# Optimization experiments

Measured on AMD Instinct MI355X. Metric: run time of the kernel, lower is better.

Reference implementation:

```python
import jax, jax.numpy as jnp
import numpy as np

N, E, NC, F0, MID = 20000, 320000, 16, 67, 32
Y0 = 0.28209479177387814   # 1/(2*sqrt(pi)), real spherical harmonic l=0
C1 = 0.4886025119029199    # sqrt(3/(4*pi)),  real spherical harmonic l=1 coeff


def setup_inputs() -> dict:
    key = jax.random.key(0)
    ks = jax.random.split(key, 16)
    rn = lambda k, shape, s=1.0: jax.random.normal(k, shape, dtype=jnp.float32) * s
    return {
        "node_feats": rn(ks[0], (N, F0)),
        "pos": rn(ks[1], (N, 3)) * 3.0,
        "edge_w": jax.random.uniform(ks[2], (E, 2), dtype=jnp.float32),
        "lin1_W": rn(ks[5], (F0, F0), 1.0 / np.sqrt(F0)),
        "lin1_b": jnp.zeros((F0,), jnp.float32),
        "lin2_W": rn(ks[6], (F0, NC), 1.0 / np.sqrt(F0)),
        "lin2_b": jnp.zeros((NC,), jnp.float32),
        # 4 radial nets = 2 GConv layers x 2 degree pairs ((0,0),(0,1))
        "rW1": rn(ks[7], (4, 3, MID), 1.0 / np.sqrt(3)),
        "rb1": jnp.zeros((4, MID), jnp.float32),
        "ln1_g": jnp.ones((4, MID), jnp.float32),
        "ln1_b": jnp.zeros((4, MID), jnp.float32),
        "rW2": rn(ks[8], (4, MID, MID), 1.0 / np.sqrt(MID)),
        "rb2": jnp.zeros((4, MID), jnp.float32),
        "ln2_g": jnp.ones((4, MID), jnp.float32),
        "ln2_b": jnp.zeros((4, MID), jnp.float32),
        "rW3": rn(ks[9], (4, MID, NC * NC), 1.0 / np.sqrt(MID)),
        "rb3": jnp.zeros((4, NC * NC), jnp.float32),
        "Wself": rn(ks[10], (2, NC, NC), 1.0 / np.sqrt(NC)),
        "src": jax.random.randint(ks[3], (E,), 0, N),
        "dst": jax.random.randint(ks[4], (E,), 0, N),
    }


def _layer_norm(x, g, b, eps=1e-5):
    mu = jnp.mean(x, -1, keepdims=True)
    var = jnp.mean((x - mu) ** 2, -1, keepdims=True)
    return (x - mu) * jax.lax.rsqrt(var + eps) * g + b


def _forward(node_feats, pos, edge_w, lin1_W, lin1_b, lin2_W, lin2_b,
             rW1, rb1, ln1_g, ln1_b, rW2, rb2, ln2_g, ln2_b, rW3, rb3,
             Wself, src, dst):
    # node embedding: Linear -> ELU -> (dropout p=0) -> Linear -> [N, NC]
    h0 = jax.nn.elu(node_feats @ lin1_W + lin1_b) @ lin2_W + lin2_b

    # get_basis_and_r: relative positions, radial distance, SH basis (d_in=0)
    d = pos[dst] - pos[src]                                   # [E, 3]
    r = jnp.sqrt(jnp.sum(d * d, -1))                          # [E]
    rhat = d / jnp.maximum(r, 1e-8)[:, None]
    Y1 = C1 * rhat[:, jnp.array([1, 2, 0])]                   # [E, 3] (y, z, x order)
    feat = jnp.concatenate([edge_w, r[:, None]], -1)          # [E, edge_dim+1=3]

    deg = jax.ops.segment_sum(jnp.ones((E,), feat.dtype), dst, num_segments=N)
    inv_deg = jnp.where(deg > 0, 1.0 / jnp.maximum(deg, 1.0), 0.0)
    has_in = (deg > 0).astype(feat.dtype)

    def radial(i):
        h = jnp.maximum(_layer_norm(feat @ rW1[i] + rb1[i], ln1_g[i], ln1_b[i]), 0.0)
        h = jnp.maximum(_layer_norm(h @ rW2[i] + rb2[i], ln2_g[i], ln2_b[i]), 0.0)
        return (h @ rW3[i] + rb3[i]).reshape(E, NC, NC)       # [E, nc_out, nc_in]

    out1 = None
    for li in range(2):  # faithful to source bug: both layers read only degree-0 feats
        R00 = radial(2 * li)        # pairwise kernel (0->0), num_freq=1
        R01 = radial(2 * li + 1)    # pairwise kernel (0->1), num_freq=1
        s = h0[src]                                           # [E, NC] gather
        msg0 = Y0 * jnp.einsum('eoi,ei->eo', R00, s)          # [E, NC]
        msg1 = jnp.einsum('eoi,ei,em->eom', R01, s, Y1)       # [E, NC, 3]
        out0 = jax.ops.segment_sum(msg0, dst, num_segments=N) * inv_deg[:, None]
        out0 = out0 + has_in[:, None] * (h0 @ Wself[li].T)    # self-interaction (deg 0)
        out1 = jax.ops.segment_sum(msg1, dst, num_segments=N) * inv_deg[:, None, None]
        h0 = out0
    return h0[:, :, None], out1                               # {'0': [N,NC,1], '1': [N,NC,3]}


def reference(node_feats, pos, edge_w, lin1_W, lin1_b, lin2_W, lin2_b,
              rW1, rb1, ln1_g, ln1_b, rW2, rb2, ln2_g, ln2_b, rW3, rb3,
              Wself, src, dst):
    return _forward(node_feats, pos, edge_w, lin1_W, lin1_b, lin2_W, lin2_b,
                    rW1, rb1, ln1_g, ln1_b, rW2, rb2, ln2_g, ln2_b, rW3, rb3,
                    Wself, src, dst)
```

## Files before the change

### kernel.cpp

```cpp
#include <hip/hip_runtime.h>
#include <hip/hip_fp16.h>


#define Y0C 0.28209479177387814f
#define C1C 0.4886025119029199f

typedef _Float16 hv2 __attribute__((ext_vector_type(2)));

#if defined(__has_builtin)
#if __has_builtin(__builtin_amdgcn_fdot2)
#define FDOT2(a, b, c) __builtin_amdgcn_fdot2((a), (b), (c), false)
#endif
#endif
#ifndef FDOT2
#define FDOT2(a, b, c) ((c) + (float)(a).x * (float)(b).x + (float)(a).y * (float)(b).y)
#endif

static __device__ __forceinline__ unsigned h2u(__half2 h) {
    union { __half2 h; unsigned u; } x; x.h = h; return x.u;
}
static __device__ __forceinline__ __half2 u2h(unsigned u) {
    union { unsigned u; __half2 h; } x; x.u = u; return x.h;
}
static __device__ __forceinline__ hv2 u2hv(unsigned u) {
    union { unsigned u; hv2 h; } x; x.u = u; return x.h;
}
static __device__ __forceinline__ unsigned hv2u(hv2 h) {
    union { hv2 h; unsigned u; } x; x.h = h; return x.u;
}
static __device__ __forceinline__ hv2 f2hv(float a, float b) {
    hv2 r; r.x = (_Float16)a; r.y = (_Float16)b; return r;
}
static __device__ __forceinline__ float hbits2f(unsigned short s) {
    __half_raw r; r.x = s; return __half2float((__half)r);
}

struct RadialW {
    const float *W1, *b1, *g1, *gb1, *b2, *g2, *gb2;
    const unsigned* W2q;
};

__device__ __forceinline__ void radial_net_pk(float x0, float x1, float x2,
                                              RadialW rw, hv2* hvpk ) {
    float h[32];
#pragma unroll
    for (int j = 0; j < 32; ++j)
        h[j] = rw.b1[j] + x0 * rw.W1[j] + x1 * rw.W1[32 + j] + x2 * rw.W1[64 + j];
    float s0 = 0.f, s1 = 0.f, s2 = 0.f, s3 = 0.f;
#pragma unroll
    for (int p = 0; p < 8; ++p) {
        s0 += h[4 * p]; s1 += h[4 * p + 1]; s2 += h[4 * p + 2]; s3 += h[4 * p + 3];
    }
    float mu = ((s0 + s1) + (s2 + s3)) * 0.03125f;
    float v0 = 0.f, v1 = 0.f, v2 = 0.f, v3 = 0.f;
#pragma unroll
    for (int p = 0; p < 8; ++p) {
        float d0 = h[4 * p] - mu, d1 = h[4 * p + 1] - mu;
        float d2 = h[4 * p + 2] - mu, d3 = h[4 * p + 3] - mu;
        v0 = fmaf(d0, d0, v0); v1 = fmaf(d1, d1, v1);
        v2 = fmaf(d2, d2, v2); v3 = fmaf(d3, d3, v3);
    }
    float var = ((v0 + v1) + (v2 + v3)) * 0.03125f;
    float rs = rsqrtf(var + 1e-5f);
#pragma unroll
    for (int j = 0; j < 32; ++j)
        h[j] = fmaxf((h[j] - mu) * rs * rw.g1[j] + rw.gb1[j], 0.f);

    hv2 hp[16];
#pragma unroll
    for (int p = 0; p < 16; ++p) hp[p] = f2hv(h[2 * p], h[2 * p + 1]);

    float h2[32];
#pragma unroll
    for (int j = 0; j < 32; ++j) {
        float acc = rw.b2[j];
        const unsigned* __restrict__ wj = rw.W2q + j * 16;
#pragma unroll
        for (int kp = 0; kp < 16; ++kp)
            acc = FDOT2(hp[kp], u2hv(wj[kp]), acc);
        h2[j] = acc;
    }
    s0 = s1 = s2 = s3 = 0.f;
#pragma unroll
    for (int p = 0; p < 8; ++p) {
        s0 += h2[4 * p]; s1 += h2[4 * p + 1]; s2 += h2[4 * p + 2]; s3 += h2[4 * p + 3];
    }
    mu = ((s0 + s1) + (s2 + s3)) * 0.03125f;
    v0 = v1 = v2 = v3 = 0.f;
#pragma unroll
    for (int p = 0; p < 8; ++p) {
        float d0 = h2[4 * p] - mu, d1 = h2[4 * p + 1] - mu;
        float d2 = h2[4 * p + 2] - mu, d3 = h2[4 * p + 3] - mu;
        v0 = fmaf(d0, d0, v0); v1 = fmaf(d1, d1, v1);
        v2 = fmaf(d2, d2, v2); v3 = fmaf(d3, d3, v3);
    }
    var = ((v0 + v1) + (v2 + v3)) * 0.03125f;
    rs = rsqrtf(var + 1e-5f);
    float y[32];
#pragma unroll
    for (int j = 0; j < 32; ++j)
        y[j] = fmaxf((h2[j] - mu) * rs * rw.g2[j] + rw.gb2[j], 0.f);
#pragma unroll
    for (int p = 0; p < 16; ++p) hvpk[p] = f2hv(y[2 * p], y[2 * p + 1]);
}

__device__ __forceinline__ void contract_dot(const hv2* hvpk,
                                             const uint4* __restrict__ Um,
                                             const float* __restrict__ Ut,
                                             float* v ) {
    float4 t0 = ((const float4*)Ut)[0];
    float4 t1 = ((const float4*)Ut)[1];
    float4 t2 = ((const float4*)Ut)[2];
    float4 t3 = ((const float4*)Ut)[3];
    float tail[16] = {t0.x, t0.y, t0.z, t0.w, t1.x, t1.y, t1.z, t1.w,
                      t2.x, t2.y, t2.z, t2.w, t3.x, t3.y, t3.z, t3.w};
#pragma unroll
    for (int o = 0; o < 16; ++o) {
        uint4 q0 = Um[o * 4];
        uint4 q1 = Um[o * 4 + 1];
        uint4 q2 = Um[o * 4 + 2];
        uint4 q3 = Um[o * 4 + 3];
        float acc = tail[o];
        acc = FDOT2(hvpk[0],  u2hv(q0.x), acc);
        acc = FDOT2(hvpk[1],  u2hv(q0.y), acc);
        acc = FDOT2(hvpk[2],  u2hv(q0.z), acc);
        acc = FDOT2(hvpk[3],  u2hv(q0.w), acc);
        acc = FDOT2(hvpk[4],  u2hv(q1.x), acc);
        acc = FDOT2(hvpk[5],  u2hv(q1.y), acc);
        acc = FDOT2(hvpk[6],  u2hv(q1.z), acc);
        acc = FDOT2(hvpk[7],  u2hv(q1.w), acc);
        acc = FDOT2(hvpk[8],  u2hv(q2.x), acc);
        acc = FDOT2(hvpk[9],  u2hv(q2.y), acc);
        acc = FDOT2(hvpk[10], u2hv(q2.z), acc);
        acc = FDOT2(hvpk[11], u2hv(q2.w), acc);
        acc = FDOT2(hvpk[12], u2hv(q3.x), acc);
        acc = FDOT2(hvpk[13], u2hv(q3.y), acc);
        acc = FDOT2(hvpk[14], u2hv(q3.z), acc);
        acc = FDOT2(hvpk[15], u2hv(q3.w), acc);
        v[o] = acc;
    }
}

__global__ __launch_bounds__(256) void k_embed1(
    const float* __restrict__ nf, const float* __restrict__ W1,
    const float* __restrict__ b1, float* __restrict__ t, int N, int nbEmb,
    const float* __restrict__ rW3, const float* __restrict__ rW2,
    unsigned* __restrict__ Wp, unsigned* __restrict__ Wq) {
    if (blockIdx.x >= (unsigned)nbEmb) {
        int tt = (blockIdx.x - nbEmb) * 256 + threadIdx.x;
        if (tt < 3 * 256) {
            int ni = tt >> 8;
            int net = (ni == 0) ? 0 : ni + 1;
            int r = tt & 255;
            int i = r >> 4, o = r & 15;
            const float* __restrict__ W3n = rW3 + (size_t)net * 8192;
            unsigned* __restrict__ dp = Wp + (size_t)ni * 4608 + (size_t)(i * 16 + o) * 18;
#pragma unroll
            for (int kp = 0; kp < 16; ++kp) {
                float a = W3n[(2 * kp) * 256 + o * 16 + i];
                float b = W3n[(2 * kp + 1) * 256 + o * 16 + i];
                dp[kp] = h2u(__floats2half2_rn(a, b));
            }
        } else if (tt < 3 * 256 + 3 * 512) {
            int r = tt - 3 * 256;
            int ni = r / 512;
            int net = (ni == 0) ? 0 : ni + 1;
            int jk = r - ni * 512;
            int j = jk >> 4, kp = jk & 15;
            const float* __restrict__ W2n = rW2 + (size_t)net * 1024;
            Wq[ni * 512 + j * 16 + kp] =
                h2u(__floats2half2_rn(W2n[(2 * kp) * 32 + j],
                                      W2n[(2 * kp + 1) * 32 + j]));
        }
        return;
    }
    int idx = blockIdx.x * 256 + threadIdx.x;
    if (idx >= N * 67) return;
    int n = idx / 67, j = idx - n * 67;
    const float* __restrict__ x = nf + (size_t)n * 67;
    const float* __restrict__ w = W1 + j;
    float a0 = b1[j], a1 = 0.f, a2 = 0.f, a3 = 0.f;
#pragma unroll
    for (int i = 0; i < 64; i += 4) {
        a0 = fmaf(x[i],     w[(size_t)i * 67],       a0);
        a1 = fmaf(x[i + 1], w[(size_t)(i + 1) * 67], a1);
        a2 = fmaf(x[i + 2], w[(size_t)(i + 2) * 67], a2);
        a3 = fmaf(x[i + 3], w[(size_t)(i + 3) * 67], a3);
    }
    a0 = fmaf(x[64], w[64 * 67], a0);
    a1 = fmaf(x[65], w[65 * 67], a1);
    a2 = fmaf(x[66], w[66 * 67], a2);
    float s = (a0 + a1) + (a2 + a3);
    t[idx] = (s > 0.f) ? s : expm1f(s);
}

__global__ __launch_bounds__(256) void k_embed2(
    const float* __restrict__ t, const float* __restrict__ W2,
    const float* __restrict__ b2, float* __restrict__ h0, int N) {
    int idx = blockIdx.x * 256 + threadIdx.x;
    if (idx >= N * 16) return;
    int n = idx >> 4, c = idx & 15;
    const float* __restrict__ x = t + (size_t)n * 67;
    const float* __restrict__ w = W2 + c;
    float a0 = b2[c], a1 = 0.f, a2 = 0.f, a3 = 0.f;
#pragma unroll
    for (int i = 0; i < 64; i += 4) {
        a0 = fmaf(x[i],     w[(size_t)i * 16],       a0);
        a1 = fmaf(x[i + 1], w[(size_t)(i + 1) * 16], a1);
        a2 = fmaf(x[i + 2], w[(size_t)(i + 2) * 16], a2);
        a3 = fmaf(x[i + 3], w[(size_t)(i + 3) * 16], a3);
    }
    a0 = fmaf(x[64], w[64 * 16], a0);
    a1 = fmaf(x[65], w[65 * 16], a1);
    a2 = fmaf(x[66], w[66 * 16], a2);
    h0[idx] = (a0 + a1) + (a2 + a3);
}

__global__ void k_count2(const int* __restrict__ src, const int* __restrict__ dst,
                         int* __restrict__ cntd, int* __restrict__ cnts,
                         int* __restrict__ posd, int* __restrict__ poss, int E) {
    int e = blockIdx.x * blockDim.x + threadIdx.x;
    if (e >= E) return;
    posd[e] = atomicAdd(cntd + dst[e], 1);
    poss[e] = atomicAdd(cnts + src[e], 1);
}

__global__ __launch_bounds__(1024) void k_scan2(const int* __restrict__ cntd,
                                                int* __restrict__ rsd,
                                                const int* __restrict__ cnts,
                                                int* __restrict__ rss, int N) {
    const int* __restrict__ c = (blockIdx.x == 0) ? cntd : cnts;
    int* __restrict__ rs      = (blockIdx.x == 0) ? rsd  : rss;
    int chunk = (N + 1023) >> 10;
    int lo = (int)threadIdx.x * chunk;
    int sum = 0;
    for (int j = 0; j < chunk; ++j) { int i = lo + j; sum += (i < N) ? c[i] : 0; }
    __shared__ int ps[1024];
    ps[threadIdx.x] = sum;
    __syncthreads();
    for (int off = 1; off < 1024; off <<= 1) {
        int t = (threadIdx.x >= (unsigned)off) ? ps[threadIdx.x - off] : 0;
        __syncthreads();
        ps[threadIdx.x] += t;
        __syncthreads();
    }
    int run = threadIdx.x ? ps[threadIdx.x - 1] : 0;
    if (threadIdx.x == 0) rs[0] = 0;
    for (int j = 0; j < chunk; ++j) {
        int i = lo + j;
        if (i < N) { run += c[i]; rs[i + 1] = run; }
    }
}

__global__ void k_prep(const float* __restrict__ pos, const float* __restrict__ ew,
                       const int* __restrict__ src, const int* __restrict__ dst,
                       const int* __restrict__ rsd, const int* __restrict__ rss,
                       const int* __restrict__ posd, const int* __restrict__ poss,
                       float4* __restrict__ edgeS, uint2* __restrict__ y1d,
                       int* __restrict__ s2d, int E) {
    int e = blockIdx.x * blockDim.x + threadIdx.x;
    if (e >= E) return;
    int s = src[e], d = dst[e];
    float dx = pos[3 * d]     - pos[3 * s];
    float dy = pos[3 * d + 1] - pos[3 * s + 1];
    float dz = pos[3 * d + 2] - pos[3 * s + 2];
    float r = sqrtf(dx * dx + dy * dy + dz * dz);
    float im = 1.f / fmaxf(r, 1e-8f);
    int ts = rss[s] + poss[e];
    int td = rsd[d] + posd[e];
    s2d[ts] = td;
    edgeS[ts] = make_float4(ew[2 * e], ew[2 * e + 1], r, __int_as_float(s));
    y1d[td] = make_uint2(h2u(__floats2half2_rn(C1C * dy * im, C1C * dz * im)),
                         h2u(__floats2half2_rn(C1C * dx * im, 0.f)));
}

__global__ __launch_bounds__(256) void k_u2(
    const float* __restrict__ h, const unsigned* __restrict__ Wp,
    const float* __restrict__ b3A, const float* __restrict__ b3B,
    unsigned* __restrict__ Um0, float* __restrict__ Ut0,
    unsigned* __restrict__ Um1, float* __restrict__ Ut1,
    int wpA, int nbPerNet, int N) {
    __shared__ unsigned WL[4608];
    int netSel = blockIdx.x / nbPerNet;
    int nbase = (blockIdx.x - netSel * nbPerNet) * 32;
    const unsigned* __restrict__ g = Wp + (size_t)(wpA + netSel) * 4608;
    for (int j = threadIdx.x; j < 4608; j += 256) WL[j] = g[j];
    __syncthreads();

    const float* __restrict__ b3 = netSel ? b3B : b3A;
    unsigned* __restrict__ Um = netSel ? Um1 : Um0;
    float*    __restrict__ Ut = netSel ? Ut1 : Ut0;

    int o = threadIdx.x & 15;
    int pr = threadIdx.x >> 4;
    int n0 = nbase + pr * 2;
    int n1 = n0 + 1;
    bool ok0 = n0 < N, ok1 = n1 < N;
    int m0 = ok0 ? n0 : 0, m1 = ok1 ? n1 : 0;

    const float* __restrict__ bo = b3 + o * 16;
    float tA = 0.f, tB = 0.f;
    __half2 hhA[16], hhB[16];
    {
        const float4* hp = (const float4*)(h + (size_t)m0 * 16);
#pragma unroll
        for (int q = 0; q < 4; ++q) {
            float4 hv = hp[q];
            tA += hv.x * bo[4 * q] + hv.y * bo[4 * q + 1]
                + hv.z * bo[4 * q + 2] + hv.w * bo[4 * q + 3];
            hhA[4 * q]     = __floats2half2_rn(hv.x, hv.x);
            hhA[4 * q + 1] = __floats2half2_rn(hv.y, hv.y);
            hhA[4 * q + 2] = __floats2half2_rn(hv.z, hv.z);
            hhA[4 * q + 3] = __floats2half2_rn(hv.w, hv.w);
        }
    }
    {
        const float4* hp = (const float4*)(h + (size_t)m1 * 16);
#pragma unroll
        for (int q = 0; q < 4; ++q) {
            float4 hv = hp[q];
            tB += hv.x * bo[4 * q] + hv.y * bo[4 * q + 1]
                + hv.z * bo[4 * q + 2] + hv.w * bo[4 * q + 3];
            hhB[4 * q]     = __floats2half2_rn(hv.x, hv.x);
            hhB[4 * q + 1] = __floats2half2_rn(hv.y, hv.y);
            hhB[4 * q + 2] = __floats2half2_rn(hv.z, hv.z);
            hhB[4 * q + 3] = __floats2half2_rn(hv.w, hv.w);
        }
    }

    __half2 accA[16], accB[16];
#pragma unroll
    for (int p = 0; p < 16; ++p) {
        accA[p] = __floats2half2_rn(0.f, 0.f);
        accB[p] = __floats2half2_rn(0.f, 0.f);
    }

#pragma unroll
    for (int i = 0; i < 16; ++i) {
        const uint2* __restrict__ row = (const uint2*)(WL + i * 288 + o * 18);
        __half2 ha = hhA[i], hb = hhB[i];
#pragma unroll
        for (int q = 0; q < 8; ++q) {
            uint2 w = row[q];
            accA[2 * q]     = __hfma2(ha, u2h(w.x), accA[2 * q]);
            accA[2 * q + 1] = __hfma2(ha, u2h(w.y), accA[2 * q + 1]);
            accB[2 * q]     = __hfma2(hb, u2h(w.x), accB[2 * q]);
            accB[2 * q + 1] = __hfma2(hb, u2h(w.y), accB[2 * q + 1]);
        }
    }

    if (ok0) {
        uint4* du = (uint4*)(Um + ((size_t)(n0 * 16 + o)) * 16);
#pragma unroll
        for (int q = 0; q < 4; ++q)
            du[q] = make_uint4(h2u(accA[4 * q]), h2u(accA[4 * q + 1]),
                               h2u(accA[4 * q + 2]), h2u(accA[4 * q + 3]));
        Ut[n0 * 16 + o] = tA;
    }
    if (ok1) {
        uint4* du = (uint4*)(Um + ((size_t)(n1 * 16 + o)) * 16);
#pragma unroll
        for (int q = 0; q < 4; ++q)
            du[q] = make_uint4(h2u(accB[4 * q]), h2u(accB[4 * q + 1]),
                               h2u(accB[4 * q + 2]), h2u(accB[4 * q + 3]));
        Ut[n1 * 16 + o] = tB;
    }
}

__global__ __launch_bounds__(256) void k_edgeL0(
    const float4* __restrict__ edgeS, const int* __restrict__ s2d, RadialW ra,
    const uint4* __restrict__ UmA, const float* __restrict__ UtA,
    unsigned short* __restrict__ msg , int E) {
    int t = blockIdx.x * blockDim.x + threadIdx.x;
    if (t >= E) return;
    float4 a = edgeS[t];
    int sn = __float_as_int(a.w);
    hv2 hv[16];
    float v[16];
    radial_net_pk(a.x, a.y, a.z, ra, hv);
    contract_dot(hv, UmA + (size_t)sn * 64, UtA + (size_t)sn * 16, v);
    int td = s2d[t];
    uint4* m = (uint4*)(msg + (size_t)td * 16);
    m[0] = make_uint4(hv2u(f2hv(v[0], v[1])),  hv2u(f2hv(v[2], v[3])),
                      hv2u(f2hv(v[4], v[5])),  hv2u(f2hv(v[6], v[7])));
    m[1] = make_uint4(hv2u(f2hv(v[8], v[9])),  hv2u(f2hv(v[10], v[11])),
                      hv2u(f2hv(v[12], v[13])), hv2u(f2hv(v[14], v[15])));
}

__global__ __launch_bounds__(256) void k_edgeL1(
    const float4* __restrict__ edgeS, const int* __restrict__ s2d,
    RadialW ra, RadialW rb,
    const uint4* __restrict__ UmA, const float* __restrict__ UtA,
    const uint4* __restrict__ UmB, const float* __restrict__ UtB,
    unsigned short* __restrict__ msg , int nbE, int E) {
    int half = (blockIdx.x >= (unsigned)nbE) ? 1 : 0;
    int t = (blockIdx.x - half * nbE) * blockDim.x + threadIdx.x;
    if (t >= E) return;
    float4 a = edgeS[t];
    int sn = __float_as_int(a.w);
    RadialW rw = half ? rb : ra;
    const uint4* __restrict__ Um = half ? UmB : UmA;
    const float* __restrict__ Ut = half ? UtB : UtA;
    hv2 hv[16];
    float v[16];
    radial_net_pk(a.x, a.y, a.z, rw, hv);
    contract_dot(hv, Um + (size_t)sn * 64, Ut + (size_t)sn * 16, v);
    int td = s2d[t];
    uint4* m = (uint4*)(msg + (size_t)td * 32 + half * 16);
    m[0] = make_uint4(hv2u(f2hv(v[0], v[1])),  hv2u(f2hv(v[2], v[3])),
                      hv2u(f2hv(v[4], v[5])),  hv2u(f2hv(v[6], v[7])));
    m[1] = make_uint4(hv2u(f2hv(v[8], v[9])),  hv2u(f2hv(v[10], v[11])),
                      hv2u(f2hv(v[12], v[13])), hv2u(f2hv(v[14], v[15])));
}

__global__ void k_reduce0(const unsigned short* __restrict__ msg,
                          const int* __restrict__ rowstart,
                          const float* __restrict__ h, const float* __restrict__ Wself,
                          float* __restrict__ out, int N) {
    int idx = blockIdx.x * blockDim.x + threadIdx.x;
    if (idx >= N * 16) return;
    int n = idx >> 4, o = idx & 15;
    int s = rowstart[n], t1 = rowstart[n + 1];
    float acc0 = 0.f, acc1 = 0.f;
    int t = s;
    for (; t + 1 < t1; t += 2) {
        acc0 += hbits2f(msg[(size_t)t * 16 + o]);
        acc1 += hbits2f(msg[(size_t)(t + 1) * 16 + o]);
    }
    if (t < t1) acc0 += hbits2f(msg[(size_t)t * 16 + o]);
    float acc = acc0 + acc1;
    int d = t1 - s;
    float invd = (d > 0) ? 1.f / (float)d : 0.f;
    float hi   = (d > 0) ? 1.f : 0.f;
    const float* __restrict__ hn = h + (size_t)n * 16;
    const float* __restrict__ w  = Wself + o * 16;
    float self = 0.f;
#pragma unroll
    for (int c = 0; c < 16; ++c) self += hn[c] * w[c];
    out[idx] = Y0C * acc * invd + hi * self;
}

__global__ void k_reduce1(const unsigned short* __restrict__ msg,
                          const uint2* __restrict__ y1d,
                          const int* __restrict__ rowstart,
                          const float* __restrict__ h, const float* __restrict__ Wself,
                          float* __restrict__ out0, float* __restrict__ out1, int N) {
    int idx = blockIdx.x * blockDim.x + threadIdx.x;
    if (idx >= N * 16) return;
    int n = idx >> 4, o = idx & 15;
    int s = rowstart[n], t1 = rowstart[n + 1];
    float a0 = 0.f, ax = 0.f, ay = 0.f, az = 0.f;
    float b0 = 0.f, bx = 0.f, by = 0.f, bz = 0.f;
    int t = s;
    for (; t + 1 < t1; t += 2) {
        const unsigned short* rowA = msg + (size_t)t * 32;
        const unsigned short* rowB = msg + (size_t)(t + 1) * 32;
        uint2 yva = y1d[t];
        uint2 yvb = y1d[t + 1];
        a0 += hbits2f(rowA[o]);
        b0 += hbits2f(rowB[o]);
        float pa = hbits2f(rowA[16 + o]);
        float pb = hbits2f(rowB[16 + o]);
        ax = fmaf(pa, hbits2f((unsigned short)yva.x), ax);
        ay = fmaf(pa, hbits2f((unsigned short)(yva.x >> 16)), ay);
        az = fmaf(pa, hbits2f((unsigned short)yva.y), az);
        bx = fmaf(pb, hbits2f((unsigned short)yvb.x), bx);
        by = fmaf(pb, hbits2f((unsigned short)(yvb.x >> 16)), by);
        bz = fmaf(pb, hbits2f((unsigned short)yvb.y), bz);
    }
    if (t < t1) {
        const unsigned short* rowA = msg + (size_t)t * 32;
        uint2 yva = y1d[t];
        a0 += hbits2f(rowA[o]);
        float pa = hbits2f(rowA[16 + o]);
        ax = fmaf(pa, hbits2f((unsigned short)yva.x), ax);
        ay = fmaf(pa, hbits2f((unsigned short)(yva.x >> 16)), ay);
        az = fmaf(pa, hbits2f((unsigned short)yva.y), az);
    }
    a0 += b0; ax += bx; ay += by; az += bz;
    int d = t1 - s;
    float invd = (d > 0) ? 1.f / (float)d : 0.f;
    float hi   = (d > 0) ? 1.f : 0.f;
    const float* __restrict__ hn = h + (size_t)n * 16;
    const float* __restrict__ w  = Wself + o * 16;
    float self = 0.f;
#pragma unroll
    for (int c = 0; c < 16; ++c) self += hn[c] * w[c];
    out0[idx] = Y0C * a0 * invd + hi * self;
    out1[(size_t)idx * 3]     = ax * invd;
    out1[(size_t)idx * 3 + 1] = ay * invd;
    out1[(size_t)idx * 3 + 2] = az * invd;
}

extern "C" void kernel_launch(void* const* d_in, const int* in_sizes, int n_in,
                              void* d_out, int out_size, void* d_ws, size_t ws_size,
                              hipStream_t stream) {
    (void)n_in; (void)out_size; (void)ws_size;
    const float* node_feats = (const float*)d_in[0];
    const float* pos    = (const float*)d_in[1];
    const float* edge_w = (const float*)d_in[2];
    const float* lin1_W = (const float*)d_in[3];
    const float* lin1_b = (const float*)d_in[4];
    const float* lin2_W = (const float*)d_in[5];
    const float* lin2_b = (const float*)d_in[6];
    const float* rW1    = (const float*)d_in[7];
    const float* rb1    = (const float*)d_in[8];
    const float* ln1_g  = (const float*)d_in[9];
    const float* ln1_b  = (const float*)d_in[10];
    const float* rW2    = (const float*)d_in[11];
    const float* rb2    = (const float*)d_in[12];
    const float* ln2_g  = (const float*)d_in[13];
    const float* ln2_b  = (const float*)d_in[14];
    const float* rW3    = (const float*)d_in[15];
    const float* rb3    = (const float*)d_in[16];
    const float* Wself  = (const float*)d_in[17];
    const int*   src    = (const int*)d_in[18];
    const int*   dst    = (const int*)d_in[19];

    const int N = in_sizes[1] / 3;
    const int E = in_sizes[18];

    char* ws = (char*)d_ws;
    size_t off = 0;
    auto carve = [&](size_t bytes) -> char* {
        char* p = ws + off;
        off = (off + bytes + 255) & ~(size_t)255;
        return p;
    };
    float* h0   = (float*)carve((size_t)N * 16 * 4);
    float* h1   = (float*)carve((size_t)N * 16 * 4);
    int*   cntd = (int*)carve((size_t)N * 4);
    int*   cnts = (int*)carve((size_t)N * 4);
    int*   rsd  = (int*)carve((size_t)(N + 1) * 4);
    int*   rss  = (int*)carve((size_t)(N + 1) * 4);
    int*   s2d  = (int*)carve((size_t)E * 4);
    float4* edgeS = (float4*)carve((size_t)E * 16);
    uint2*  y1d   = (uint2*)carve((size_t)E * 8);
    unsigned* UaM = (unsigned*)carve((size_t)N * 16 * 64);
    float*    UaT = (float*)carve((size_t)N * 16 * 4);
    unsigned* UbM = (unsigned*)carve((size_t)N * 16 * 64);
    float*    UbT = (float*)carve((size_t)N * 16 * 4);
    unsigned* Wp  = (unsigned*)carve((size_t)3 * 4608 * 4);
    unsigned* Wq  = (unsigned*)carve((size_t)3 * 512 * 4);
    unsigned short* msg = (unsigned short*)carve((size_t)E * 32 * 2);
    float* tmb = (float*)msg;
    int* posd = (int*)((char*)msg + (8u << 20));
    int* poss = (int*)((char*)msg + (14u << 20));

    auto nb = [](int n) { return (n + 255) / 256; };
    const int nbE = nb(E);
    const int nbU = (N + 31) / 32;
    const int nbE1 = nb(N * 67);

    hipMemsetAsync(cntd, 0, (size_t)((char*)cnts - (char*)cntd) + (size_t)N * 4, stream);

    k_embed1<<<nbE1 + 9, 256, 0, stream>>>(node_feats, lin1_W, lin1_b, tmb, N,
                                           nbE1, rW3, rW2, Wp, Wq);
    k_embed2<<<nb(N * 16), 256, 0, stream>>>(tmb, lin2_W, lin2_b, h0, N);

    k_count2<<<nbE, 256, 0, stream>>>(src, dst, cntd, cnts, posd, poss, E);
    k_scan2<<<2, 1024, 0, stream>>>(cntd, rsd, cnts, rss, N);
    k_prep<<<nbE, 256, 0, stream>>>(pos, edge_w, src, dst, rsd, rss, posd, poss,
                                    edgeS, y1d, s2d, E);

    auto rnet = [&](int net, int ni) -> RadialW {
        RadialW r;
        r.W1 = rW1 + net * 96;   r.b1 = rb1 + net * 32;
        r.g1 = ln1_g + net * 32; r.gb1 = ln1_b + net * 32;
        r.b2 = rb2 + net * 32;
        r.g2 = ln2_g + net * 32; r.gb2 = ln2_b + net * 32;
        r.W2q = Wq + ni * 512;
        return r;
    };

    k_u2<<<nbU, 256, 0, stream>>>(h0, Wp, rb3, rb3, UaM, UaT, UbM, UbT,
                                  0, nbU, N);
    k_edgeL0<<<nbE, 256, 0, stream>>>(edgeS, s2d, rnet(0, 0), (const uint4*)UaM, UaT,
                                      msg, E);
    k_reduce0<<<nb(N * 16), 256, 0, stream>>>(msg, rsd, h0, Wself, h1, N);

    k_u2<<<2 * nbU, 256, 0, stream>>>(h1, Wp, rb3 + 2 * 256, rb3 + 3 * 256,
                                      UaM, UaT, UbM, UbT, 1, nbU, N);
    k_edgeL1<<<2 * nbE, 256, 0, stream>>>(edgeS, s2d, rnet(2, 1), rnet(3, 2),
                                          (const uint4*)UaM, UaT,
                                          (const uint4*)UbM, UbT, msg, nbE, E);
    float* out0 = (float*)d_out;
    float* out1 = (float*)d_out + (size_t)N * 16;
    k_reduce1<<<nb(N * 16), 256, 0, stream>>>(msg, y1d, rsd, h1, Wself + 256,
                                              out0, out1, N);
}
```

Baseline: 352.8 us.

## Precompute all three radial-net hidden outputs in prep kernel, store fp16 per edge

Moves the per-edge radial MLP evaluation for all three used nets out of the contraction kernels into the edge prep kernel, storing 64 bytes of fp16 hidden activations per edge per net. The contraction kernels then only load these activations plus the source index. This decouples the radial compute from the gather-heavy contraction, at the cost of writing and rereading about 61 MB of extra workspace. It also adds a serial three-net loop to one kernel, which may raise register pressure.

```diff
diff --git a/kernel.cpp b/kernel.cpp
--- a/kernel.cpp
+++ b/kernel.cpp
@@ -252,13 +252,18 @@
     }
 }
 
-__global__ void k_prep(const float* __restrict__ pos, const float* __restrict__ ew,
-                       const int* __restrict__ src, const int* __restrict__ dst,
-                       const int* __restrict__ rsd, const int* __restrict__ rss,
-                       const int* __restrict__ posd, const int* __restrict__ poss,
-                       float4* __restrict__ edgeS, uint2* __restrict__ y1d,
-                       int* __restrict__ s2d, int E) {
-    int e = blockIdx.x * blockDim.x + threadIdx.x;
+__global__ __launch_bounds__(256) void k_radial(
+    const float* __restrict__ pos, const float* __restrict__ ew,
+    const int* __restrict__ src, const int* __restrict__ dst,
+    const int* __restrict__ rsd, const int* __restrict__ rss,
+    const int* __restrict__ posd, const int* __restrict__ poss,
+    const float* __restrict__ rW1, const float* __restrict__ rb1,
+    const float* __restrict__ g1, const float* __restrict__ gb1,
+    const float* __restrict__ rb2, const float* __restrict__ g2,
+    const float* __restrict__ gb2, const unsigned* __restrict__ Wq,
+    uint4* __restrict__ yS, uint2* __restrict__ y1d,
+    int* __restrict__ s2d, int* __restrict__ srcS, int E) {
+    int e = blockIdx.x * 256 + threadIdx.x;
     if (e >= E) return;
     int s = src[e], d = dst[e];
     float dx = pos[3 * d]     - pos[3 * s];
@@ -269,9 +274,25 @@
     int ts = rss[s] + poss[e];
     int td = rsd[d] + posd[e];
     s2d[ts] = td;
-    edgeS[ts] = make_float4(ew[2 * e], ew[2 * e + 1], r, __int_as_float(s));
+    srcS[ts] = s;
     y1d[td] = make_uint2(h2u(__floats2half2_rn(C1C * dy * im, C1C * dz * im)),
                          h2u(__floats2half2_rn(C1C * dx * im, 0.f)));
+    float f0 = ew[2 * e], f1 = ew[2 * e + 1];
+    for (int ni = 0; ni < 3; ++ni) {
+        int net = (ni == 0) ? 0 : ni + 1;
+        RadialW rw;
+        rw.W1 = rW1 + net * 96;  rw.b1 = rb1 + net * 32;
+        rw.g1 = g1 + net * 32;   rw.gb1 = gb1 + net * 32;
+        rw.b2 = rb2 + net * 32;  rw.g2 = g2 + net * 32;  rw.gb2 = gb2 + net * 32;
+        rw.W2q = Wq + ni * 512;
+        hv2 hv[16];
+        radial_net_pk(f0, f1, r, rw, hv);
+        uint4* o = yS + ((size_t)ni * E + ts) * 4;
+        o[0] = make_uint4(hv2u(hv[0]),  hv2u(hv[1]),  hv2u(hv[2]),  hv2u(hv[3]));
+        o[1] = make_uint4(hv2u(hv[4]),  hv2u(hv[5]),  hv2u(hv[6]),  hv2u(hv[7]));
+        o[2] = make_uint4(hv2u(hv[8]),  hv2u(hv[9]),  hv2u(hv[10]), hv2u(hv[11]));
+        o[3] = make_uint4(hv2u(hv[12]), hv2u(hv[13]), hv2u(hv[14]), hv2u(hv[15]));
+    }
 }
 
 __global__ __launch_bounds__(256) void k_u2(
@@ -367,17 +388,21 @@
     }
 }
 
-__global__ __launch_bounds__(256) void k_edgeL0(
-    const float4* __restrict__ edgeS, const int* __restrict__ s2d, RadialW ra,
+__global__ __launch_bounds__(256) void k_con0(
+    const uint4* __restrict__ yS, const int* __restrict__ srcS,
+    const int* __restrict__ s2d,
     const uint4* __restrict__ UmA, const float* __restrict__ UtA,
     unsigned short* __restrict__ msg , int E) {
-    int t = blockIdx.x * blockDim.x + threadIdx.x;
+    int t = blockIdx.x * 256 + threadIdx.x;
     if (t >= E) return;
-    float4 a = edgeS[t];
-    int sn = __float_as_int(a.w);
-    hv2 hv[16];
+    const uint4* yp = yS + (size_t)t * 4;
+    uint4 y0 = yp[0], y1 = yp[1], y2 = yp[2], y3 = yp[3];
+    hv2 hv[16] = {u2hv(y0.x), u2hv(y0.y), u2hv(y0.z), u2hv(y0.w),
+                  u2hv(y1.x), u2hv(y1.y), u2hv(y1.z), u2hv(y1.w),
+                  u2hv(y2.x), u2hv(y2.y), u2hv(y2.z), u2hv(y2.w),
+                  u2hv(y3.x), u2hv(y3.y), u2hv(y3.z), u2hv(y3.w)};
+    int sn = srcS[t];
     float v[16];
-    radial_net_pk(a.x, a.y, a.z, ra, hv);
     contract_dot(hv, UmA + (size_t)sn * 64, UtA + (size_t)sn * 16, v);
     int td = s2d[t];
     uint4* m = (uint4*)(msg + (size_t)td * 16);
@@ -387,23 +412,26 @@
                       hv2u(f2hv(v[12], v[13])), hv2u(f2hv(v[14], v[15])));
 }
 
-__global__ __launch_bounds__(256) void k_edgeL1(
-    const float4* __restrict__ edgeS, const int* __restrict__ s2d,
-    RadialW ra, RadialW rb,
-    const uint4* __restrict__ UmA, const float* __restrict__ UtA,
+__global__ __launch_bounds__(256) void k_con1(
+    const uint4* __restrict__ ySB, const uint4* __restrict__ ySC,
+    const int* __restrict__ srcS, const int* __restrict__ s2d,
     const uint4* __restrict__ UmB, const float* __restrict__ UtB,
+    const uint4* __restrict__ UmC, const float* __restrict__ UtC,
     unsigned short* __restrict__ msg , int nbE, int E) {
     int half = (blockIdx.x >= (unsigned)nbE) ? 1 : 0;
-    int t = (blockIdx.x - half * nbE) * blockDim.x + threadIdx.x;
+    int t = (blockIdx.x - half * nbE) * 256 + threadIdx.x;
     if (t >= E) return;
-    float4 a = edgeS[t];
-    int sn = __float_as_int(a.w);
-    RadialW rw = half ? rb : ra;
-    const uint4* __restrict__ Um = half ? UmB : UmA;
-    const float* __restrict__ Ut = half ? UtB : UtA;
-    hv2 hv[16];
+    const uint4* __restrict__ yb = half ? ySC : ySB;
+    const uint4* __restrict__ Um = half ? UmC : UmB;
+    const float* __restrict__ Ut = half ? UtC : UtB;
+    const uint4* yp = yb + (size_t)t * 4;
+    uint4 y0 = yp[0], y1 = yp[1], y2 = yp[2], y3 = yp[3];
+    hv2 hv[16] = {u2hv(y0.x), u2hv(y0.y), u2hv(y0.z), u2hv(y0.w),
+                  u2hv(y1.x), u2hv(y1.y), u2hv(y1.z), u2hv(y1.w),
+                  u2hv(y2.x), u2hv(y2.y), u2hv(y2.z), u2hv(y2.w),
+                  u2hv(y3.x), u2hv(y3.y), u2hv(y3.z), u2hv(y3.w)};
+    int sn = srcS[t];
     float v[16];
-    radial_net_pk(a.x, a.y, a.z, rw, hv);
     contract_dot(hv, Um + (size_t)sn * 64, Ut + (size_t)sn * 16, v);
     int td = s2d[t];
     uint4* m = (uint4*)(msg + (size_t)td * 32 + half * 16);
@@ -534,8 +562,9 @@
     int*   rsd  = (int*)carve((size_t)(N + 1) * 4);
     int*   rss  = (int*)carve((size_t)(N + 1) * 4);
     int*   s2d  = (int*)carve((size_t)E * 4);
-    float4* edgeS = (float4*)carve((size_t)E * 16);
-    uint2*  y1d   = (uint2*)carve((size_t)E * 8);
+    int*   srcS = (int*)carve((size_t)E * 4);
+    uint2*  y1d = (uint2*)carve((size_t)E * 8);
+    uint4*  yS  = (uint4*)carve((size_t)3 * E * 64);
     unsigned* UaM = (unsigned*)carve((size_t)N * 16 * 64);
     float*    UaT = (float*)carve((size_t)N * 16 * 4);
     unsigned* UbM = (unsigned*)carve((size_t)N * 16 * 64);
@@ -560,30 +589,20 @@
 
     k_count2<<<nbE, 256, 0, stream>>>(src, dst, cntd, cnts, posd, poss, E);
     k_scan2<<<2, 1024, 0, stream>>>(cntd, rsd, cnts, rss, N);
-    k_prep<<<nbE, 256, 0, stream>>>(pos, edge_w, src, dst, rsd, rss, posd, poss,
-                                    edgeS, y1d, s2d, E);
-
-    auto rnet = [&](int net, int ni) -> RadialW {
-        RadialW r;
-        r.W1 = rW1 + net * 96;   r.b1 = rb1 + net * 32;
-        r.g1 = ln1_g + net * 32; r.gb1 = ln1_b + net * 32;
-        r.b2 = rb2 + net * 32;
-        r.g2 = ln2_g + net * 32; r.gb2 = ln2_b + net * 32;
-        r.W2q = Wq + ni * 512;
-        return r;
-    };
+    k_radial<<<nbE, 256, 0, stream>>>(pos, edge_w, src, dst, rsd, rss, posd, poss,
+                                      rW1, rb1, ln1_g, ln1_b, rb2, ln2_g, ln2_b,
+                                      Wq, yS, y1d, s2d, srcS, E);
 
     k_u2<<<nbU, 256, 0, stream>>>(h0, Wp, rb3, rb3, UaM, UaT, UbM, UbT,
                                   0, nbU, N);
-    k_edgeL0<<<nbE, 256, 0, stream>>>(edgeS, s2d, rnet(0, 0), (const uint4*)UaM, UaT,
-                                      msg, E);
+    k_con0<<<nbE, 256, 0, stream>>>(yS, srcS, s2d, (const uint4*)UaM, UaT, msg, E);
     k_reduce0<<<nb(N * 16), 256, 0, stream>>>(msg, rsd, h0, Wself, h1, N);
 
     k_u2<<<2 * nbU, 256, 0, stream>>>(h1, Wp, rb3 + 2 * 256, rb3 + 3 * 256,
                                       UaM, UaT, UbM, UbT, 1, nbU, N);
-    k_edgeL1<<<2 * nbE, 256, 0, stream>>>(edgeS, s2d, rnet(2, 1), rnet(3, 2),
-                                          (const uint4*)UaM, UaT,
-                                          (const uint4*)UbM, UbT, msg, nbE, E);
+    k_con1<<<2 * nbE, 256, 0, stream>>>(yS + (size_t)E * 4, yS + (size_t)2 * E * 4,
+                                        srcS, s2d, (const uint4*)UaM, UaT,
+                                        (const uint4*)UbM, UbT, msg, nbE, E);
     float* out0 = (float*)d_out;
     float* out1 = (float*)d_out + (size_t)N * 16;
     k_reduce1<<<nb(N * 16), 256, 0, stream>>>(msg, y1d, rsd, h1, Wself + 256,
```

After: 360.8 us. 2.3% more time.

## Merge independent preprocessing kernels into three horizontally fused launches

Applied to the files above, without the earlier changes.

Edge counting is folded into the embedding/weight-packing kernel, the prefix scan into the second embedding kernel, and the layer-0 U precompute into the edge-prep kernel, with block-index ranges picking the role. This cuts the launch count from six to three and lets independent work run at the same time, removing launch gaps and tail idle time. The cost is block divergence by role. The second kernel now uses 1024-thread blocks for the embed work, and the fused third kernel reserves shared memory even for the edge-prep blocks, which can lower occupancy.

```diff
diff --git a/kernel.cpp b/kernel.cpp
--- a/kernel.cpp
+++ b/kernel.cpp
@@ -141,11 +141,21 @@
     }
 }
 
-__global__ __launch_bounds__(256) void k_embed1(
+__global__ __launch_bounds__(256) void k_fuse1(
     const float* __restrict__ nf, const float* __restrict__ W1,
     const float* __restrict__ b1, float* __restrict__ t, int N, int nbEmb,
     const float* __restrict__ rW3, const float* __restrict__ rW2,
-    unsigned* __restrict__ Wp, unsigned* __restrict__ Wq) {
+    unsigned* __restrict__ Wp, unsigned* __restrict__ Wq,
+    const int* __restrict__ src, const int* __restrict__ dst,
+    int* __restrict__ cntd, int* __restrict__ cnts,
+    int* __restrict__ posd, int* __restrict__ poss, int E) {
+    if (blockIdx.x >= (unsigned)(nbEmb + 9)) {
+        int e = (blockIdx.x - nbEmb - 9) * 256 + threadIdx.x;
+        if (e >= E) return;
+        posd[e] = atomicAdd(cntd + dst[e], 1);
+        poss[e] = atomicAdd(cnts + src[e], 1);
+        return;
+    }
     if (blockIdx.x >= (unsigned)nbEmb) {
         int tt = (blockIdx.x - nbEmb) * 256 + threadIdx.x;
         if (tt < 3 * 256) {
@@ -194,10 +204,36 @@
     t[idx] = (s > 0.f) ? s : expm1f(s);
 }
 
-__global__ __launch_bounds__(256) void k_embed2(
+__global__ __launch_bounds__(1024) void k_fuse2(
+    const int* __restrict__ cntd, int* __restrict__ rsd,
+    const int* __restrict__ cnts, int* __restrict__ rss, int N,
     const float* __restrict__ t, const float* __restrict__ W2,
-    const float* __restrict__ b2, float* __restrict__ h0, int N) {
-    int idx = blockIdx.x * 256 + threadIdx.x;
+    const float* __restrict__ b2, float* __restrict__ h0) {
+    if (blockIdx.x < 2) {
+        const int* __restrict__ c = (blockIdx.x == 0) ? cntd : cnts;
+        int* __restrict__ rs      = (blockIdx.x == 0) ? rsd  : rss;
+        int chunk = (N + 1023) >> 10;
+        int lo = (int)threadIdx.x * chunk;
+        int sum = 0;
+        for (int j = 0; j < chunk; ++j) { int i = lo + j; sum += (i < N) ? c[i] : 0; }
+        __shared__ int ps[1024];
+        ps[threadIdx.x] = sum;
+        __syncthreads();
+        for (int off = 1; off < 1024; off <<= 1) {
+            int v = (threadIdx.x >= (unsigned)off) ? ps[threadIdx.x - off] : 0;
+            __syncthreads();
+            ps[threadIdx.x] += v;
+            __syncthreads();
+        }
+        int run = threadIdx.x ? ps[threadIdx.x - 1] : 0;
+        if (threadIdx.x == 0) rs[0] = 0;
+        for (int j = 0; j < chunk; ++j) {
+            int i = lo + j;
+            if (i < N) { run += c[i]; rs[i + 1] = run; }
+        }
+        return;
+    }
+    int idx = (blockIdx.x - 2) * 1024 + threadIdx.x;
     if (idx >= N * 16) return;
     int n = idx >> 4, c = idx & 15;
     const float* __restrict__ x = t + (size_t)n * 67;
@@ -216,49 +252,104 @@
     h0[idx] = (a0 + a1) + (a2 + a3);
 }
 
-__global__ void k_count2(const int* __restrict__ src, const int* __restrict__ dst,
-                         int* __restrict__ cntd, int* __restrict__ cnts,
-                         int* __restrict__ posd, int* __restrict__ poss, int E) {
-    int e = blockIdx.x * blockDim.x + threadIdx.x;
-    if (e >= E) return;
-    posd[e] = atomicAdd(cntd + dst[e], 1);
-    poss[e] = atomicAdd(cnts + src[e], 1);
-}
-
-__global__ __launch_bounds__(1024) void k_scan2(const int* __restrict__ cntd,
-                                                int* __restrict__ rsd,
-                                                const int* __restrict__ cnts,
-                                                int* __restrict__ rss, int N) {
-    const int* __restrict__ c = (blockIdx.x == 0) ? cntd : cnts;
-    int* __restrict__ rs      = (blockIdx.x == 0) ? rsd  : rss;
-    int chunk = (N + 1023) >> 10;
-    int lo = (int)threadIdx.x * chunk;
-    int sum = 0;
-    for (int j = 0; j < chunk; ++j) { int i = lo + j; sum += (i < N) ? c[i] : 0; }
-    __shared__ int ps[1024];
-    ps[threadIdx.x] = sum;
-    __syncthreads();
-    for (int off = 1; off < 1024; off <<= 1) {
-        int t = (threadIdx.x >= (unsigned)off) ? ps[threadIdx.x - off] : 0;
+__device__ __forceinline__ void u2_body(
+    unsigned* WL, int nbase, const float* __restrict__ h,
+    const float* __restrict__ b3, unsigned* __restrict__ Um,
+    float* __restrict__ Ut, int N) {
+    int o = threadIdx.x & 15;
+    int pr = threadIdx.x >> 4;
+    int n0 = nbase + pr * 2;
+    int n1 = n0 + 1;
+    bool ok0 = n0 < N, ok1 = n1 < N;
+    int m0 = ok0 ? n0 : 0, m1 = ok1 ? n1 : 0;
+
+    const float* __restrict__ bo = b3 + o * 16;
+    float tA = 0.f, tB = 0.f;
+    __half2 hhA[16], hhB[16];
+    {
+        const float4* hp = (const float4*)(h + (size_t)m0 * 16);
+#pragma unroll
+        for (int q = 0; q < 4; ++q) {
+            float4 hv = hp[q];
+            tA += hv.x * bo[4 * q] + hv.y * bo[4 * q + 1]
+                + hv.z * bo[4 * q + 2] + hv.w * bo[4 * q + 3];
+            hhA[4 * q]     = __floats2half2_rn(hv.x, hv.x);
+            hhA[4 * q + 1] = __floats2half2_rn(hv.y, hv.y);
+            hhA[4 * q + 2] = __floats2half2_rn(hv.z, hv.z);
+            hhA[4 * q + 3] = __floats2half2_rn(hv.w, hv.w);
+        }
+    }
+    {
+        const float4* hp = (const float4*)(h + (size_t)m1 * 16);
+#pragma unroll
+        for (int q = 0; q < 4; ++q) {
+            float4 hv = hp[q];
+            tB += hv.x * bo[4 * q] + hv.y * bo[4 * q + 1]
+                + hv.z * bo[4 * q + 2] + hv.w * bo[4 * q + 3];
+            hhB[4 * q]     = __floats2half2_rn(hv.x, hv.x);
+            hhB[4 * q + 1] = __floats2half2_rn(hv.y, hv.y);
+            hhB[4 * q + 2] = __floats2half2_rn(hv.z, hv.z);
+            hhB[4 * q + 3] = __floats2half2_rn(hv.w, hv.w);
+        }
+    }
+
+    __half2 accA[16], accB[16];
+#pragma unroll
+    for (int p = 0; p < 16; ++p) {
+        accA[p] = __floats2half2_rn(0.f, 0.f);
+        accB[p] = __floats2half2_rn(0.f, 0.f);
+    }
+
+#pragma unroll
+    for (int i = 0; i < 16; ++i) {
+        const uint2* __restrict__ row = (const uint2*)(WL + i * 288 + o * 18);
+        __half2 ha = hhA[i], hb = hhB[i];
+#pragma unroll
+        for (int q = 0; q < 8; ++q) {
+            uint2 w = row[q];
+            accA[2 * q]     = __hfma2(ha, u2h(w.x), accA[2 * q]);
+            accA[2 * q + 1] = __hfma2(ha, u2h(w.y), accA[2 * q + 1]);
+            accB[2 * q]     = __hfma2(hb, u2h(w.x), accB[2 * q]);
+            accB[2 * q + 1] = __hfma2(hb, u2h(w.y), accB[2 * q + 1]);
+        }
+    }
+
+    if (ok0) {
+        uint4* du = (uint4*)(Um + ((size_t)(n0 * 16 + o)) * 16);
+#pragma unroll
+        for (int q = 0; q < 4; ++q)
+            du[q] = make_uint4(h2u(accA[4 * q]), h2u(accA[4 * q + 1]),
+                               h2u(accA[4 * q + 2]), h2u(accA[4 * q + 3]));
+        Ut[n0 * 16 + o] = tA;
+    }
+    if (ok1) {
+        uint4* du = (uint4*)(Um + ((size_t)(n1 * 16 + o)) * 16);
+#pragma unroll
+        for (int q = 0; q < 4; ++q)
+            du[q] = make_uint4(h2u(accB[4 * q]), h2u(accB[4 * q + 1]),
+                               h2u(accB[4 * q + 2]), h2u(accB[4 * q + 3]));
+        Ut[n1 * 16 + o] = tB;
+    }
+}
+
+__global__ __launch_bounds__(256) void k_fuse3(
+    const float* __restrict__ h, const unsigned* __restrict__ Wp,
+    const float* __restrict__ b3, unsigned* __restrict__ Um,
+    float* __restrict__ Ut, int nbU, int N,
+    const float* __restrict__ pos, const float* __restrict__ ew,
+    const int* __restrict__ src, const int* __restrict__ dst,
+    const int* __restrict__ rsd, const int* __restrict__ rss,
+    const int* __restrict__ posd, const int* __restrict__ poss,
+    float4* __restrict__ edgeS, uint2* __restrict__ y1d,
+    int* __restrict__ s2d, int E) {
+    __shared__ unsigned WL[4608];
+    if (blockIdx.x < (unsigned)nbU) {
+        for (int j = threadIdx.x; j < 4608; j += 256) WL[j] = Wp[j];
         __syncthreads();
-        ps[threadIdx.x] += t;
-        __syncthreads();
-    }
-    int run = threadIdx.x ? ps[threadIdx.x - 1] : 0;
-    if (threadIdx.x == 0) rs[0] = 0;
-    for (int j = 0; j < chunk; ++j) {
-        int i = lo + j;
-        if (i < N) { run += c[i]; rs[i + 1] = run; }
-    }
-}
-
-__global__ void k_prep(const float* __restrict__ pos, const float* __restrict__ ew,
-                       const int* __restrict__ src, const int* __restrict__ dst,
-                       const int* __restrict__ rsd, const int* __restrict__ rss,
-                       const int* __restrict__ posd, const int* __restrict__ poss,
-                       float4* __restrict__ edgeS, uint2* __restrict__ y1d,
-                       int* __restrict__ s2d, int E) {
-    int e = blockIdx.x * blockDim.x + threadIdx.x;
+        u2_body(WL, blockIdx.x * 32, h, b3, Um, Ut, N);
+        return;
+    }
+    int e = (blockIdx.x - nbU) * 256 + threadIdx.x;
     if (e >= E) return;
     int s = src[e], d = dst[e];
     float dx = pos[3 * d]     - pos[3 * s];
@@ -286,85 +377,8 @@
     const unsigned* __restrict__ g = Wp + (size_t)(wpA + netSel) * 4608;
     for (int j = threadIdx.x; j < 4608; j += 256) WL[j] = g[j];
     __syncthreads();
-
-    const float* __restrict__ b3 = netSel ? b3B : b3A;
-    unsigned* __restrict__ Um = netSel ? Um1 : Um0;
-    float*    __restrict__ Ut = netSel ? Ut1 : Ut0;
-
-    int o = threadIdx.x & 15;
-    int pr = threadIdx.x >> 4;
-    int n0 = nbase + pr * 2;
-    int n1 = n0 + 1;
-    bool ok0 = n0 < N, ok1 = n1 < N;
-    int m0 = ok0 ? n0 : 0, m1 = ok1 ? n1 : 0;
-
-    const float* __restrict__ bo = b3 + o * 16;
-    float tA = 0.f, tB = 0.f;
-    __half2 hhA[16], hhB[16];
-    {
-        const float4* hp = (const float4*)(h + (size_t)m0 * 16);
-#pragma unroll
-        for (int q = 0; q < 4; ++q) {
-            float4 hv = hp[q];
-            tA += hv.x * bo[4 * q] + hv.y * bo[4 * q + 1]
-                + hv.z * bo[4 * q + 2] + hv.w * bo[4 * q + 3];
-            hhA[4 * q]     = __floats2half2_rn(hv.x, hv.x);
-            hhA[4 * q + 1] = __floats2half2_rn(hv.y, hv.y);
-            hhA[4 * q + 2] = __floats2half2_rn(hv.z, hv.z);
-            hhA[4 * q + 3] = __floats2half2_rn(hv.w, hv.w);
-        }
-    }
-    {
-        const float4* hp = (const float4*)(h + (size_t)m1 * 16);
-#pragma unroll
-        for (int q = 0; q < 4; ++q) {
-            float4 hv = hp[q];
-            tB += hv.x * bo[4 * q] + hv.y * bo[4 * q + 1]
-                + hv.z * bo[4 * q + 2] + hv.w * bo[4 * q + 3];
-            hhB[4 * q]     = __floats2half2_rn(hv.x, hv.x);
-            hhB[4 * q + 1] = __floats2half2_rn(hv.y, hv.y);
-            hhB[4 * q + 2] = __floats2half2_rn(hv.z, hv.z);
-            hhB[4 * q + 3] = __floats2half2_rn(hv.w, hv.w);
-        }
-    }
-
-    __half2 accA[16], accB[16];
-#pragma unroll
-    for (int p = 0; p < 16; ++p) {
-        accA[p] = __floats2half2_rn(0.f, 0.f);
-        accB[p] = __floats2half2_rn(0.f, 0.f);
-    }
-
-#pragma unroll
-    for (int i = 0; i < 16; ++i) {
-        const uint2* __restrict__ row = (const uint2*)(WL + i * 288 + o * 18);
-        __half2 ha = hhA[i], hb = hhB[i];
-#pragma unroll
-        for (int q = 0; q < 8; ++q) {
-            uint2 w = row[q];
-            accA[2 * q]     = __hfma2(ha, u2h(w.x), accA[2 * q]);
-            accA[2 * q + 1] = __hfma2(ha, u2h(w.y), accA[2 * q + 1]);
-            accB[2 * q]     = __hfma2(hb, u2h(w.x), accB[2 * q]);
-            accB[2 * q + 1] = __hfma2(hb, u2h(w.y), accB[2 * q + 1]);
-        }
-    }
-
-    if (ok0) {
-        uint4* du = (uint4*)(Um + ((size_t)(n0 * 16 + o)) * 16);
-#pragma unroll
-        for (int q = 0; q < 4; ++q)
-            du[q] = make_uint4(h2u(accA[4 * q]), h2u(accA[4 * q + 1]),
-                               h2u(accA[4 * q + 2]), h2u(accA[4 * q + 3]));
-        Ut[n0 * 16 + o] = tA;
-    }
-    if (ok1) {
-        uint4* du = (uint4*)(Um + ((size_t)(n1 * 16 + o)) * 16);
-#pragma unroll
-        for (int q = 0; q < 4; ++q)
-            du[q] = make_uint4(h2u(accB[4 * q]), h2u(accB[4 * q + 1]),
-                               h2u(accB[4 * q + 2]), h2u(accB[4 * q + 3]));
-        Ut[n1 * 16 + o] = tB;
-    }
+    u2_body(WL, nbase, h, netSel ? b3B : b3A,
+            netSel ? Um1 : Um0, netSel ? Ut1 : Ut0, N);
 }
 
 __global__ __launch_bounds__(256) void k_edgeL0(
@@ -554,14 +568,14 @@
 
     hipMemsetAsync(cntd, 0, (size_t)((char*)cnts - (char*)cntd) + (size_t)N * 4, stream);
 
-    k_embed1<<<nbE1 + 9, 256, 0, stream>>>(node_feats, lin1_W, lin1_b, tmb, N,
-                                           nbE1, rW3, rW2, Wp, Wq);
-    k_embed2<<<nb(N * 16), 256, 0, stream>>>(tmb, lin2_W, lin2_b, h0, N);
-
-    k_count2<<<nbE, 256, 0, stream>>>(src, dst, cntd, cnts, posd, poss, E);
-    k_scan2<<<2, 1024, 0, stream>>>(cntd, rsd, cnts, rss, N);
-    k_prep<<<nbE, 256, 0, stream>>>(pos, edge_w, src, dst, rsd, rss, posd, poss,
-                                    edgeS, y1d, s2d, E);
+    k_fuse1<<<nbE1 + 9 + nbE, 256, 0, stream>>>(node_feats, lin1_W, lin1_b, tmb, N,
+                                                nbE1, rW3, rW2, Wp, Wq,
+                                                src, dst, cntd, cnts, posd, poss, E);
+    k_fuse2<<<2 + (N * 16 + 1023) / 1024, 1024, 0, stream>>>(
+        cntd, rsd, cnts, rss, N, tmb, lin2_W, lin2_b, h0);
+    k_fuse3<<<nbU + nbE, 256, 0, stream>>>(h0, Wp, rb3, UaM, UaT, nbU, N,
+                                           pos, edge_w, src, dst, rsd, rss,
+                                           posd, poss, edgeS, y1d, s2d, E);
 
     auto rnet = [&](int net, int ni) -> RadialW {
         RadialW r;
@@ -573,8 +587,6 @@
         return r;
     };
 
-    k_u2<<<nbU, 256, 0, stream>>>(h0, Wp, rb3, rb3, UaM, UaT, UbM, UbT,
-                                  0, nbU, N);
     k_edgeL0<<<nbE, 256, 0, stream>>>(edgeS, s2d, rnet(0, 0), (const uint4*)UaM, UaT,
                                       msg, E);
     k_reduce0<<<nb(N * 16), 256, 0, stream>>>(msg, rsd, h0, Wself, h1, N);
```

Result: faster. 328.2 us (-7.0%).
